# Kernel tuning notes

Measured on AMD Instinct MI355X. Metric: run time of the kernel, lower is better.

Reference implementation:

```python
import jax, jax.numpy as jnp
import numpy as np

DEPTH, DIM, DFF, VOCAB = 4, 512, 2048, 4096
EPS = 1e-5

def layernorm(x, w, b):
    mu = jnp.mean(x, axis=-1, keepdims=True)
    var = jnp.mean((x - mu) ** 2, axis=-1, keepdims=True)
    return (x - mu) * jax.lax.rsqrt(var + EPS) * w + b

def sconv(x, phazor_c, last_conv_c):
    # x: [B,L,dim] real; phazor_c, last_conv_c: [dim] complex
    B, L, D = x.shape
    r = jnp.abs(phazor_c)
    p = jnp.tanh(r) * jnp.exp(1j * jnp.angle(phazor_c))          # [dim]
    prog = p[None, :] ** jnp.arange(L, dtype=jnp.float32)[:, None]  # [L,dim]
    filt_fft = jnp.fft.fft(prog, n=2 * L, axis=0)                # [2L,dim]
    x_fft = jnp.fft.fft(x.astype(jnp.complex64), n=2 * L, axis=1)  # [B,2L,dim]
    conv = jnp.fft.ifft(filt_fft[None] * x_fft, axis=1)[:, :L]   # [B,L,dim]
    conv = conv + last_conv_c[None, None, :] * prog[None] * p[None, None, :]
    return conv.real.astype(x.dtype)

def setup_inputs() -> dict:
    key = jax.random.key(0)
    ks = jax.random.split(key, 20)
    f32 = jnp.float32
    inp = {}
    inp['x'] = jax.random.normal(ks[0], (2, 4096, VOCAB), dtype=f32)
    inp['Win'] = jax.random.normal(ks[1], (DIM, VOCAB), dtype=f32) * VOCAB ** -0.5
    inp['bin'] = jnp.zeros((DIM,), f32)
    inp['ln1_w'] = jnp.ones((DEPTH, DIM), f32)
    inp['ln1_b'] = jnp.zeros((DEPTH, DIM), f32)
    # phazor init: exp(2*pi*i*arange/dim)*|randn|
    ang = 2 * np.pi * jnp.arange(DIM, dtype=f32) / DIM
    mag = jnp.abs(jax.random.normal(ks[2], (DEPTH, DIM), dtype=f32))
    inp['phz_re'] = mag * jnp.cos(ang)[None]
    inp['phz_im'] = mag * jnp.sin(ang)[None]
    inp['lc_re'] = jax.random.normal(ks[3], (DEPTH, DIM), dtype=f32)
    inp['lc_im'] = jax.random.normal(ks[4], (DEPTH, DIM), dtype=f32)
    inp['sc_lin'] = jnp.ones((DEPTH, DIM), f32)
    inp['ln2_w'] = jnp.ones((DEPTH, DIM), f32)
    inp['ln2_b'] = jnp.zeros((DEPTH, DIM), f32)
    inp['W1'] = jax.random.normal(ks[5], (DEPTH, DFF, DIM), dtype=f32) * DIM ** -0.5
    inp['b1'] = jnp.zeros((DEPTH, DFF), f32)
    inp['W2'] = jax.random.normal(ks[6], (DEPTH, DIM, DFF), dtype=f32) * DFF ** -0.5
    inp['b2'] = jnp.zeros((DEPTH, DIM), f32)
    inp['lnl_w'] = jnp.ones((DIM,), f32)
    inp['lnl_b'] = jnp.zeros((DIM,), f32)
    inp['Wout'] = jax.random.normal(ks[7], (VOCAB, DIM), dtype=f32) * DIM ** -0.5
    inp['bout'] = jnp.zeros((VOCAB,), f32)
    return inp

def _forward(x, Win, bin, ln1_w, ln1_b, phz_re, phz_im, lc_re, lc_im, sc_lin,
             ln2_w, ln2_b, W1, b1, W2, b2, lnl_w, lnl_b, Wout, bout):
    h = jnp.einsum('blv,dv->bld', x, Win) + bin  # token_in

    def body(h, p):
        l1w, l1b, pr, pi, lr, li, scl, l2w, l2b, w1, b1_, w2, b2_ = p
        y = jax.nn.silu(layernorm(h, l1w, l1b))
        y = sconv(y, pr + 1j * pi, lr + 1j * li)
        h = h + y * scl
        y = layernorm(h, l2w, l2b)
        y = jax.nn.silu(jnp.einsum('bld,fd->blf', y, w1) + b1_)
        y = jnp.einsum('blf,df->bld', y, w2) + b2_
        return h + y, None

    xs = (ln1_w, ln1_b, phz_re, phz_im, lc_re, lc_im, sc_lin,
          ln2_w, ln2_b, W1, b1, W2, b2)
    h, _ = jax.lax.scan(body, h, xs)
    h = layernorm(h, lnl_w, lnl_b)
    return jnp.einsum('bld,vd->blv', h, Wout) + bout

def reference(x, Win, bin, ln1_w, ln1_b, phz_re, phz_im, lc_re, lc_im, sc_lin,
              ln2_w, ln2_b, W1, b1, W2, b2, lnl_w, lnl_b, Wout, bout):
    return _forward(x, Win, bin, ln1_w, ln1_b, phz_re, phz_im, lc_re, lc_im,
                    sc_lin, ln2_w, ln2_b, W1, b1, W2, b2, lnl_w, lnl_b, Wout, bout)
```

## Files before the change

### kernel.cpp

```cpp
#include <hip/hip_runtime.h>
#include <hip/hip_bf16.h>
#include <cstdint>
#include <cstddef>

#define DEPTH 4
#define DIM 512
#define DFF 2048
#define VOCAB 4096
#define NB 2
#define LSEQ 4096
#define MR (NB*LSEQ)
#define EPSL 1e-5f
#define NC 256
#define TCH 16

typedef __attribute__((ext_vector_type(8))) short  s8v;
typedef __attribute__((ext_vector_type(4))) float  f4v;
typedef __attribute__((ext_vector_type(8))) __bf16 bf8v;

__device__ __forceinline__ unsigned short f2b(float f) {
  union { float f; unsigned int u; } v; v.f = f;
  unsigned int r = v.u + 0x7FFFu + ((v.u >> 16) & 1u);
  return (unsigned short)(r >> 16);
}

__device__ __forceinline__ void gld16(const void* g, void* l) {
  __builtin_amdgcn_global_load_lds(
      (const __attribute__((address_space(1))) unsigned int*)(uintptr_t)g,
      (__attribute__((address_space(3))) unsigned int*)(uintptr_t)l,
      16, 0, 0);
}

template<int N> __device__ __forceinline__ void wvm() {
  if constexpr (N == 8)      asm volatile("s_waitcnt vmcnt(8)" ::: "memory");
  else if constexpr (N == 6) asm volatile("s_waitcnt vmcnt(6)" ::: "memory");
  else if constexpr (N == 4) asm volatile("s_waitcnt vmcnt(4)" ::: "memory");
  else if constexpr (N == 3) asm volatile("s_waitcnt vmcnt(3)" ::: "memory");
  else                       asm volatile("s_waitcnt vmcnt(0)" ::: "memory");
}

__device__ __forceinline__ void wred64(float& s, float& s2) {
#pragma unroll
  for (int off = 32; off; off >>= 1) { s += __shfl_xor(s, off, 64); s2 += __shfl_xor(s2, off, 64); }
}

__global__ void __launch_bounds__(256) cvt_f32_bf16(
    const float* __restrict__ in, unsigned short* __restrict__ out, int n8)
{
  int i = blockIdx.x * 256 + threadIdx.x;
  if (i >= n8) return;
  const f4v* p = (const f4v*)(in + (size_t)i * 8);
  f4v a = p[0], b = p[1];
  s8v o;
  o[0]=(short)f2b(a[0]); o[1]=(short)f2b(a[1]); o[2]=(short)f2b(a[2]); o[3]=(short)f2b(a[3]);
  o[4]=(short)f2b(b[0]); o[5]=(short)f2b(b[1]); o[6]=(short)f2b(b[2]); o[7]=(short)f2b(b[3]);
  *(s8v*)(out + (size_t)i * 8) = o;
}

__device__ __forceinline__ void phz2p(float re, float im, float& pre, float& pim) {
  float r = sqrtf(re * re + im * im);
  float t = (r > 1e-20f) ? (tanhf(r) / r) : 1.0f;
  pre = t * re; pim = t * im;
}

__global__ void __launch_bounds__(512) ln_scan(
    const float* __restrict__ h,
    const float* __restrict__ lnw, const float* __restrict__ lnb,
    const float* __restrict__ pr, const float* __restrict__ pi,
    float* __restrict__ y, float* __restrict__ stA)
{
  __shared__ float ls[TCH][DIM];
  const int d = threadIdx.x;
  const int c = blockIdx.x, b = blockIdx.y;
  const size_t rbase = ((size_t)b * LSEQ + (size_t)c * TCH) * DIM + d;
#pragma unroll 4
  for (int j = 0; j < TCH; ++j) ls[j][d] = h[rbase + (size_t)j * DIM];
  __syncthreads();
  const int wave = threadIdx.x >> 6, lane = threadIdx.x & 63;
  const int c8 = lane * 8;
  f4v w0 = *(const f4v*)(lnw + c8), w1 = *(const f4v*)(lnw + c8 + 4);
  f4v b0 = *(const f4v*)(lnb + c8), b1 = *(const f4v*)(lnb + c8 + 4);
#pragma unroll
  for (int jj = 0; jj < 2; ++jj) {
    int j = wave * 2 + jj;
    f4v v0 = *(const f4v*)&ls[j][c8];
    f4v v1 = *(const f4v*)&ls[j][c8 + 4];
    float s = 0.f, s2 = 0.f;
#pragma unroll
    for (int q = 0; q < 4; ++q) { s += v0[q]; s2 += v0[q]*v0[q]; s += v1[q]; s2 += v1[q]*v1[q]; }
    wred64(s, s2);
    float mu = s * (1.f / DIM);
    float rs = rsqrtf(s2 * (1.f / DIM) - mu * mu + EPSL);
    f4v o0, o1;
#pragma unroll
    for (int q = 0; q < 4; ++q) {
      float a = (v0[q] - mu) * rs * w0[q] + b0[q];
      o0[q] = a / (1.f + __expf(-a));
      float e = (v1[q] - mu) * rs * w1[q] + b1[q];
      o1[q] = e / (1.f + __expf(-e));
    }
    *(f4v*)&ls[j][c8]     = o0;
    *(f4v*)&ls[j][c8 + 4] = o1;
    size_t yo = ((size_t)b * LSEQ + (size_t)c * TCH + j) * DIM + c8;
    *(f4v*)(y + yo)     = o0;
    *(f4v*)(y + yo + 4) = o1;
  }
  __syncthreads();
  float pre, pim; phz2p(pr[d], pi[d], pre, pim);
  float sre = 0.f, sim = 0.f;
#pragma unroll
  for (int j = 0; j < TCH; ++j) {
    float xv = ls[j][d];
    float nre = fmaf(pre, sre, fmaf(-pim, sim, xv));
    float nim = fmaf(pre, sim, pim * sre);
    sre = nre; sim = nim;
  }
  size_t o = (((size_t)b * NC + c) * DIM + d) * 2;
  stA[o] = sre; stA[o + 1] = sim;
}

__global__ void __launch_bounds__(256) scan_b(
    const float* __restrict__ stA, float* __restrict__ carry,
    const float* __restrict__ pr, const float* __restrict__ pi,
    const float* __restrict__ lcr, const float* __restrict__ lci)
{
  int idx = blockIdx.x * 256 + threadIdx.x;
  int b = idx >> 9, d = idx & (DIM - 1);
  float pre, pim; phz2p(pr[d], pi[d], pre, pim);
  float qre = pre, qim = pim;
#pragma unroll
  for (int t = 0; t < 4; ++t) { float nr = qre*qre - qim*qim; float ni = 2.f*qre*qim; qre = nr; qim = ni; }
  float cre = lcr[d], cim = lci[d];
  const size_t base = (size_t)b * NC * DIM * 2 + (size_t)d * 2;
  for (int c0 = 0; c0 < NC; c0 += 8) {
    float ar[8], ai[8];
#pragma unroll
    for (int k = 0; k < 8; ++k) {
      size_t o = base + (size_t)(c0 + k) * DIM * 2;
      ar[k] = stA[o]; ai[k] = stA[o + 1];
    }
#pragma unroll
    for (int k = 0; k < 8; ++k) {
      size_t o = base + (size_t)(c0 + k) * DIM * 2;
      carry[o] = cre; carry[o + 1] = cim;
      float nr = fmaf(qre, cre, fmaf(-qim, cim, ar[k]));
      float ni = fmaf(qre, cim, fmaf(qim, cre, ai[k]));
      cre = nr; cim = ni;
    }
  }
}

__global__ void __launch_bounds__(512) scan_c_ln2(
    const float* __restrict__ y, float* __restrict__ h, const float* __restrict__ carry,
    const float* __restrict__ pr, const float* __restrict__ pi,
    const float* __restrict__ scl,
    const float* __restrict__ lnw, const float* __restrict__ lnb,
    unsigned short* __restrict__ yb)
{
  __shared__ float ls[TCH][DIM];
  const int d = threadIdx.x;
  const int c = blockIdx.x, b = blockIdx.y;
  float pre, pim; phz2p(pr[d], pi[d], pre, pim);
  size_t co = (((size_t)b * NC + c) * DIM + d) * 2;
  float sre = carry[co], sim = carry[co + 1];
  const float sc = scl[d];
  const size_t rbase = ((size_t)b * LSEQ + (size_t)c * TCH) * DIM + d;
#pragma unroll 4
  for (int j = 0; j < TCH; ++j) {
    size_t o = rbase + (size_t)j * DIM;
    float xv = y[o];
    float nre = fmaf(pre, sre, fmaf(-pim, sim, xv));
    float nim = fmaf(pre, sim, pim * sre);
    sre = nre; sim = nim;
    float hv = h[o] + sre * sc;
    h[o] = hv;
    ls[j][d] = hv;
  }
  __syncthreads();
  const int wave = threadIdx.x >> 6, lane = threadIdx.x & 63;
  const int c8 = lane * 8;
  f4v w0 = *(const f4v*)(lnw + c8), w1 = *(const f4v*)(lnw + c8 + 4);
  f4v b0 = *(const f4v*)(lnb + c8), b1 = *(const f4v*)(lnb + c8 + 4);
#pragma unroll
  for (int jj = 0; jj < 2; ++jj) {
    int j = wave * 2 + jj;
    f4v v0 = *(const f4v*)&ls[j][c8];
    f4v v1 = *(const f4v*)&ls[j][c8 + 4];
    float s = 0.f, s2 = 0.f;
#pragma unroll
    for (int q = 0; q < 4; ++q) { s += v0[q]; s2 += v0[q]*v0[q]; s += v1[q]; s2 += v1[q]*v1[q]; }
    wred64(s, s2);
    float mu = s * (1.f / DIM);
    float rs = rsqrtf(s2 * (1.f / DIM) - mu * mu + EPSL);
    s8v o;
#pragma unroll
    for (int q = 0; q < 4; ++q) {
      o[q]     = (short)f2b((v0[q] - mu) * rs * w0[q] + b0[q]);
      o[4 + q] = (short)f2b((v1[q] - mu) * rs * w1[q] + b1[q]);
    }
    *(s8v*)(yb + ((size_t)b * LSEQ + (size_t)c * TCH + j) * DIM + c8) = o;
  }
}

__global__ void __launch_bounds__(512) ln_final(
    const float* __restrict__ h,
    const float* __restrict__ lnw, const float* __restrict__ lnb,
    unsigned short* __restrict__ yb)
{
  __shared__ float ls[TCH][DIM];
  const int d = threadIdx.x;
  const int c = blockIdx.x, b = blockIdx.y;
  const size_t rbase = ((size_t)b * LSEQ + (size_t)c * TCH) * DIM + d;
#pragma unroll 4
  for (int j = 0; j < TCH; ++j) ls[j][d] = h[rbase + (size_t)j * DIM];
  __syncthreads();
  const int wave = threadIdx.x >> 6, lane = threadIdx.x & 63;
  const int c8 = lane * 8;
  f4v w0 = *(const f4v*)(lnw + c8), w1 = *(const f4v*)(lnw + c8 + 4);
  f4v b0 = *(const f4v*)(lnb + c8), b1 = *(const f4v*)(lnb + c8 + 4);
#pragma unroll
  for (int jj = 0; jj < 2; ++jj) {
    int j = wave * 2 + jj;
    f4v v0 = *(const f4v*)&ls[j][c8];
    f4v v1 = *(const f4v*)&ls[j][c8 + 4];
    float s = 0.f, s2 = 0.f;
#pragma unroll
    for (int q = 0; q < 4; ++q) { s += v0[q]; s2 += v0[q]*v0[q]; s += v1[q]; s2 += v1[q]*v1[q]; }
    wred64(s, s2);
    float mu = s * (1.f / DIM);
    float rs = rsqrtf(s2 * (1.f / DIM) - mu * mu + EPSL);
    s8v o;
#pragma unroll
    for (int q = 0; q < 4; ++q) {
      o[q]     = (short)f2b((v0[q] - mu) * rs * w0[q] + b0[q]);
      o[4 + q] = (short)f2b((v1[q] - mu) * rs * w1[q] + b1[q]);
    }
    *(s8v*)(yb + ((size_t)b * LSEQ + (size_t)c * TCH + j) * DIM + c8) = o;
  }
}

template<int EPI, int BN>
__global__ void __launch_bounds__(256, BN == 64 ? 4 : 3) gemm_p(
    const unsigned short* __restrict__ A, const unsigned short* __restrict__ Bm,
    const float* __restrict__ bias,
    float* __restrict__ Cf, unsigned short* __restrict__ Cb,
    int N, int K, int lda, int ldb)
{
  constexpr int WN  = BN / 2;
  constexpr int NJ  = WN / 16;
  constexpr int VPT = 2 + BN / 64;
  __shared__ unsigned short As[3][128 * 32];
  __shared__ unsigned short Bs[3][BN * 32];
  const int tid  = threadIdx.x;
  const int lane = tid & 63, wave = tid >> 6;
  const int wm = wave >> 1, wn = wave & 1;
  const int fr = lane & 15, fq = lane >> 4;

  int bx, by;
  {
    int gx = gridDim.x;
    int nwg = gx * gridDim.y;
    int b = blockIdx.y * gx + blockIdx.x;
    int lid = (b & 7) * (nwg >> 3) + (b >> 3);
    bx = lid % gx; by = lid / gx;
  }
  const int m0 = by * 128, n0 = bx * BN;
  const int nkt = K >> 5;

  f4v acc[4][NJ];
#pragma unroll
  for (int i = 0; i < 4; ++i)
#pragma unroll
    for (int j = 0; j < NJ; ++j) acc[i][j] = (f4v){0.f, 0.f, 0.f, 0.f};

  const int row2 = tid >> 2, col2 = (tid & 3) << 3;
  auto stage = [&](int buf, int kt) {
    const unsigned short* Ab = A  + (size_t)m0 * lda + kt * 32;
    const unsigned short* Bb = Bm + (size_t)n0 * ldb + kt * 32;
    gld16(Ab + (size_t)row2 * lda + col2,        &As[buf][tid * 8]);
    gld16(Ab + (size_t)(row2 + 64) * lda + col2, &As[buf][(256 + tid) * 8]);
    gld16(Bb + (size_t)row2 * ldb + col2,        &Bs[buf][tid * 8]);
    if constexpr (BN == 128)
      gld16(Bb + (size_t)(row2 + 64) * ldb + col2, &Bs[buf][(256 + tid) * 8]);
  };

  stage(0, 0);
  stage(1, 1);

  int b0 = 0, b1 = 1, b2 = 2;
  for (int kt = 0; kt < nkt; ++kt) {
    bool pf = (kt + 2 < nkt);
    if (pf) stage(b2, kt + 2);
    if (pf)                    wvm<2 * VPT>();
    else if (kt + 1 < nkt)     wvm<VPT>();
    else                       wvm<0>();
    __builtin_amdgcn_s_barrier();
    __builtin_amdgcn_sched_barrier(0);
    bf8v av[4], bv[NJ];
#pragma unroll
    for (int i = 0; i < 4; ++i)
      av[i] = *(const bf8v*)&As[b0][(wm * 64 + i * 16 + fr) * 32 + fq * 8];
#pragma unroll
    for (int j = 0; j < NJ; ++j)
      bv[j] = *(const bf8v*)&Bs[b0][(wn * WN + j * 16 + fr) * 32 + fq * 8];
#pragma unroll
    for (int i = 0; i < 4; ++i)
#pragma unroll
      for (int j = 0; j < NJ; ++j)
        acc[i][j] = __builtin_amdgcn_mfma_f32_16x16x32_bf16(av[i], bv[j], acc[i][j], 0, 0, 0);
    __builtin_amdgcn_sched_barrier(0);
    __builtin_amdgcn_s_barrier();
    int t = b0; b0 = b1; b1 = b2; b2 = t;
  }

#pragma unroll
  for (int j = 0; j < NJ; ++j) {
    const int col = n0 + wn * WN + j * 16 + fr;
    const float bsv = bias[col];
#pragma unroll
    for (int i = 0; i < 4; ++i) {
#pragma unroll
      for (int r = 0; r < 4; ++r) {
        const int row = m0 + wm * 64 + i * 16 + fq * 4 + r;
        const size_t off = (size_t)row * N + col;
        float v = acc[i][j][r] + bsv;
        if constexpr (EPI == 0) {
          Cf[off] = v;
        } else if constexpr (EPI == 1) {
          float sv = v / (1.f + __expf(-v));
          Cb[off] = f2b(sv);
        } else {
          Cf[off] = Cf[off] + v;
        }
      }
    }
  }
}

extern "C" void kernel_launch(void* const* d_in, const int* in_sizes, int n_in,
                              void* d_out, int out_size, void* d_ws, size_t ws_size,
                              hipStream_t stream)
{
  (void)in_sizes; (void)n_in; (void)out_size; (void)ws_size;
  const float* x    = (const float*)d_in[0];
  const float* Win  = (const float*)d_in[1];
  const float* bin  = (const float*)d_in[2];
  const float* ln1w = (const float*)d_in[3];
  const float* ln1b = (const float*)d_in[4];
  const float* phzr = (const float*)d_in[5];
  const float* phzi = (const float*)d_in[6];
  const float* lcr  = (const float*)d_in[7];
  const float* lci  = (const float*)d_in[8];
  const float* scl  = (const float*)d_in[9];
  const float* ln2w = (const float*)d_in[10];
  const float* ln2b = (const float*)d_in[11];
  const float* W1   = (const float*)d_in[12];
  const float* b1   = (const float*)d_in[13];
  const float* W2   = (const float*)d_in[14];
  const float* b2   = (const float*)d_in[15];
  const float* lnlw = (const float*)d_in[16];
  const float* lnlb = (const float*)d_in[17];
  const float* Wout = (const float*)d_in[18];
  const float* bout = (const float*)d_in[19];

  char* wsp = (char*)d_ws;
  auto alloc = [&](size_t bytes) { char* p = wsp; wsp += (bytes + 255) & ~(size_t)255; return p; };
  float*          h     = (float*)alloc((size_t)MR * DIM * 4);
  float*          y     = (float*)alloc((size_t)MR * DIM * 4);
  unsigned short* yb    = (unsigned short*)alloc((size_t)MR * DIM * 2);
  unsigned short* Winb  = (unsigned short*)alloc((size_t)DIM * VOCAB * 2);
  unsigned short* W1b   = (unsigned short*)alloc((size_t)DEPTH * DFF * DIM * 2);
  unsigned short* W2b   = (unsigned short*)alloc((size_t)DEPTH * DIM * DFF * 2);
  unsigned short* Woutb = (unsigned short*)alloc((size_t)VOCAB * DIM * 2);
  float*          stA   = (float*)alloc((size_t)NB * NC * DIM * 2 * 4);
  float*          carry = (float*)alloc((size_t)NB * NC * DIM * 2 * 4);

  unsigned short* xb   = (unsigned short*)d_out;
  unsigned short* act1 = (unsigned short*)d_out;

  dim3 blk(256);
  dim3 fblk(512);
  dim3 fgrid(NC, NB);
  cvt_f32_bf16<<<dim3(((size_t)MR * VOCAB) / 2048), blk, 0, stream>>>(x, xb, (int)(((size_t)MR * VOCAB) / 8));
  cvt_f32_bf16<<<dim3((DIM * VOCAB) / 2048), blk, 0, stream>>>(Win, Winb, DIM * VOCAB / 8);
  cvt_f32_bf16<<<dim3((DEPTH * DFF * DIM) / 2048), blk, 0, stream>>>(W1, W1b, DEPTH * DFF * DIM / 8);
  cvt_f32_bf16<<<dim3((DEPTH * DFF * DIM) / 2048), blk, 0, stream>>>(W2, W2b, DEPTH * DIM * DFF / 8);
  cvt_f32_bf16<<<dim3((VOCAB * DIM) / 2048), blk, 0, stream>>>(Wout, Woutb, VOCAB * DIM / 8);

  gemm_p<0, 64><<<dim3(DIM / 64, MR / 128), blk, 0, stream>>>(
      xb, Winb, bin, h, nullptr, DIM, VOCAB, VOCAB, VOCAB);
  ln_scan<<<fgrid, fblk, 0, stream>>>(h, ln1w, ln1b, phzr, phzi, y, stA);

  for (int l = 0; l < DEPTH; ++l) {
    scan_b<<<dim3((NB * DIM) / 256), blk, 0, stream>>>(stA, carry, phzr + l * DIM, phzi + l * DIM,
                                                       lcr + l * DIM, lci + l * DIM);
    scan_c_ln2<<<fgrid, fblk, 0, stream>>>(y, h, carry, phzr + l * DIM, phzi + l * DIM,
                                           scl + l * DIM, ln2w + l * DIM, ln2b + l * DIM, yb);
    gemm_p<1, 128><<<dim3(DFF / 128, MR / 128), blk, 0, stream>>>(
        yb, W1b + (size_t)l * DFF * DIM, b1 + l * DFF, nullptr, act1, DFF, DIM, DIM, DIM);
    gemm_p<2, 64><<<dim3(DIM / 64, MR / 128), blk, 0, stream>>>(
        act1, W2b + (size_t)l * DIM * DFF, b2 + l * DIM, h, nullptr, DIM, DFF, DFF, DFF);
    if (l < DEPTH - 1) {
      ln_scan<<<fgrid, fblk, 0, stream>>>(h, ln1w + (l + 1) * DIM, ln1b + (l + 1) * DIM,
                                          phzr + (l + 1) * DIM, phzi + (l + 1) * DIM, y, stA);
    }
  }
  ln_final<<<fgrid, fblk, 0, stream>>>(h, lnlw, lnlb, yb);
  gemm_p<0, 128><<<dim3(VOCAB / 128, MR / 128), blk, 0, stream>>>(
      yb, Woutb, bout, (float*)d_out, nullptr, VOCAB, DIM, DIM, DIM);
}
```

Baseline: 584.3 us.

## Fuse fp32-to-bf16 input conversion into token-in GEMM loading fp32 tiles

```diff
diff --git a/kernel.cpp b/kernel.cpp
--- a/kernel.cpp
+++ b/kernel.cpp
@@ -32,8 +32,10 @@
 }
 
 template<int N> __device__ __forceinline__ void wvm() {
-  if constexpr (N == 8)      asm volatile("s_waitcnt vmcnt(8)" ::: "memory");
+  if constexpr (N == 10)     asm volatile("s_waitcnt vmcnt(10)" ::: "memory");
+  else if constexpr (N == 8) asm volatile("s_waitcnt vmcnt(8)" ::: "memory");
   else if constexpr (N == 6) asm volatile("s_waitcnt vmcnt(6)" ::: "memory");
+  else if constexpr (N == 5) asm volatile("s_waitcnt vmcnt(5)" ::: "memory");
   else if constexpr (N == 4) asm volatile("s_waitcnt vmcnt(4)" ::: "memory");
   else if constexpr (N == 3) asm volatile("s_waitcnt vmcnt(3)" ::: "memory");
   else                       asm volatile("s_waitcnt vmcnt(0)" ::: "memory");
@@ -332,6 +334,100 @@
         } else {
           Cf[off] = Cf[off] + v;
         }
+      }
+    }
+  }
+}
+
+__global__ void __launch_bounds__(256, 2) gemm_tok(
+    const float* __restrict__ A, const unsigned short* __restrict__ Bm,
+    const float* __restrict__ bias, float* __restrict__ Cf, int N, int K)
+{
+  constexpr int VPT = 5;
+  __shared__ float          Asf[3][128 * 32];
+  __shared__ unsigned short Bs[3][64 * 32];
+  const int tid  = threadIdx.x;
+  const int lane = tid & 63, wave = tid >> 6;
+  const int wm = wave >> 1, wn = wave & 1;
+  const int fr = lane & 15, fq = lane >> 4;
+
+  int bx, by;
+  {
+    int gx = gridDim.x;
+    int nwg = gx * gridDim.y;
+    int b = blockIdx.y * gx + blockIdx.x;
+    int lid = (b & 7) * (nwg >> 3) + (b >> 3);
+    bx = lid % gx; by = lid / gx;
+  }
+  const int m0 = by * 128, n0 = bx * 64;
+  const int nkt = K >> 5;
+
+  f4v acc[4][2];
+#pragma unroll
+  for (int i = 0; i < 4; ++i)
+#pragma unroll
+    for (int j = 0; j < 2; ++j) acc[i][j] = (f4v){0.f, 0.f, 0.f, 0.f};
+
+  const int row2 = tid >> 2, col2 = (tid & 3) << 3;
+  auto stage = [&](int buf, int kt) {
+    const float* Ab = A + (size_t)m0 * K + kt * 32;
+    const unsigned short* Bb = Bm + (size_t)n0 * K + kt * 32;
+#pragma unroll
+    for (int q = 0; q < 4; ++q) {
+      int s = q * 256 + tid;
+      int row = s >> 3;
+      int c4  = (s & 7) ^ (row & 7);
+      gld16(Ab + (size_t)row * K + c4 * 4, &Asf[buf][s * 4]);
+    }
+    gld16(Bb + (size_t)row2 * K + col2, &Bs[buf][tid * 8]);
+  };
+
+  stage(0, 0);
+  stage(1, 1);
+
+  int b0 = 0, b1 = 1, b2 = 2;
+  for (int kt = 0; kt < nkt; ++kt) {
+    bool pf = (kt + 2 < nkt);
+    if (pf) stage(b2, kt + 2);
+    if (pf)                    wvm<2 * VPT>();
+    else if (kt + 1 < nkt)     wvm<VPT>();
+    else                       wvm<0>();
+    __builtin_amdgcn_s_barrier();
+    __builtin_amdgcn_sched_barrier(0);
+    bf8v av[4], bv[2];
+#pragma unroll
+    for (int i = 0; i < 4; ++i) {
+      int arow = wm * 64 + i * 16 + fr;
+      int g0 = arow * 8 + ((fq * 2) ^ (arow & 7));
+      int g1 = g0 ^ 1;
+      f4v lo = *(const f4v*)&Asf[b0][g0 * 4];
+      f4v hi = *(const f4v*)&Asf[b0][g1 * 4];
+#pragma unroll
+      for (int q = 0; q < 4; ++q) { av[i][q] = (__bf16)lo[q]; av[i][4 + q] = (__bf16)hi[q]; }
+    }
+#pragma unroll
+    for (int j = 0; j < 2; ++j)
+      bv[j] = *(const bf8v*)&Bs[b0][(wn * 32 + j * 16 + fr) * 32 + fq * 8];
+#pragma unroll
+    for (int i = 0; i < 4; ++i)
+#pragma unroll
+      for (int j = 0; j < 2; ++j)
+        acc[i][j] = __builtin_amdgcn_mfma_f32_16x16x32_bf16(av[i], bv[j], acc[i][j], 0, 0, 0);
+    __builtin_amdgcn_sched_barrier(0);
+    __builtin_amdgcn_s_barrier();
+    int t = b0; b0 = b1; b1 = b2; b2 = t;
+  }
+
+#pragma unroll
+  for (int j = 0; j < 2; ++j) {
+    const int col = n0 + wn * 32 + j * 16 + fr;
+    const float bsv = bias[col];
+#pragma unroll
+    for (int i = 0; i < 4; ++i) {
+#pragma unroll
+      for (int r = 0; r < 4; ++r) {
+        const int row = m0 + wm * 64 + i * 16 + fq * 4 + r;
+        Cf[(size_t)row * N + col] = acc[i][j][r] + bsv;
       }
     }
   }
@@ -375,20 +471,17 @@
   float*          stA   = (float*)alloc((size_t)NB * NC * DIM * 2 * 4);
   float*          carry = (float*)alloc((size_t)NB * NC * DIM * 2 * 4);
 
-  unsigned short* xb   = (unsigned short*)d_out;
   unsigned short* act1 = (unsigned short*)d_out;
 
   dim3 blk(256);
   dim3 fblk(512);
   dim3 fgrid(NC, NB);
-  cvt_f32_bf16<<<dim3(((size_t)MR * VOCAB) / 2048), blk, 0, stream>>>(x, xb, (int)(((size_t)MR * VOCAB) / 8));
   cvt_f32_bf16<<<dim3((DIM * VOCAB) / 2048), blk, 0, stream>>>(Win, Winb, DIM * VOCAB / 8);
   cvt_f32_bf16<<<dim3((DEPTH * DFF * DIM) / 2048), blk, 0, stream>>>(W1, W1b, DEPTH * DFF * DIM / 8);
   cvt_f32_bf16<<<dim3((DEPTH * DFF * DIM) / 2048), blk, 0, stream>>>(W2, W2b, DEPTH * DIM * DFF / 8);
   cvt_f32_bf16<<<dim3((VOCAB * DIM) / 2048), blk, 0, stream>>>(Wout, Woutb, VOCAB * DIM / 8);
 
-  gemm_p<0, 64><<<dim3(DIM / 64, MR / 128), blk, 0, stream>>>(
-      xb, Winb, bin, h, nullptr, DIM, VOCAB, VOCAB, VOCAB);
+  gemm_tok<<<dim3(DIM / 64, MR / 128), blk, 0, stream>>>(x, Winb, bin, h, DIM, VOCAB);
   ln_scan<<<fgrid, fblk, 0, stream>>>(h, ln1w, ln1b, phzr, phzi, y, stA);
 
   for (int l = 0; l < DEPTH; ++l) {
```

New measurement: 608.4 us. 1.04x slower.

## Split-K the input projection GEMM and fuse all bf16 conversions into one kernel

Applied to the files above, without the earlier changes.

```diff
diff --git a/kernel.cpp b/kernel.cpp
--- a/kernel.cpp
+++ b/kernel.cpp
@@ -44,17 +44,32 @@
   for (int off = 32; off; off >>= 1) { s += __shfl_xor(s, off, 64); s2 += __shfl_xor(s2, off, 64); }
 }
 
-__global__ void __launch_bounds__(256) cvt_f32_bf16(
-    const float* __restrict__ in, unsigned short* __restrict__ out, int n8)
-{
-  int i = blockIdx.x * 256 + threadIdx.x;
-  if (i >= n8) return;
-  const f4v* p = (const f4v*)(in + (size_t)i * 8);
+#define NX8 4194304
+#define NW8  262144
+#define N18  524288
+#define N28  524288
+#define NO8  262144
+__global__ void __launch_bounds__(256) cvt_all(
+    const float* __restrict__ x,  const float* __restrict__ Win,
+    const float* __restrict__ W1, const float* __restrict__ W2,
+    const float* __restrict__ Wout,
+    unsigned short* __restrict__ xb,  unsigned short* __restrict__ Winb,
+    unsigned short* __restrict__ W1b, unsigned short* __restrict__ W2b,
+    unsigned short* __restrict__ Woutb)
+{
+  long i = (long)blockIdx.x * 256 + threadIdx.x;
+  const float* src; unsigned short* dst; long j;
+  if (i < NX8)                         { src = x;    dst = xb;    j = i; }
+  else if (i < NX8 + NW8)              { src = Win;  dst = Winb;  j = i - NX8; }
+  else if (i < NX8 + NW8 + N18)        { src = W1;   dst = W1b;   j = i - NX8 - NW8; }
+  else if (i < NX8 + NW8 + N18 + N28)  { src = W2;   dst = W2b;   j = i - NX8 - NW8 - N18; }
+  else                                 { src = Wout; dst = Woutb; j = i - NX8 - NW8 - N18 - N28; }
+  const f4v* p = (const f4v*)(src + j * 8);
   f4v a = p[0], b = p[1];
   s8v o;
   o[0]=(short)f2b(a[0]); o[1]=(short)f2b(a[1]); o[2]=(short)f2b(a[2]); o[3]=(short)f2b(a[3]);
   o[4]=(short)f2b(b[0]); o[5]=(short)f2b(b[1]); o[6]=(short)f2b(b[2]); o[7]=(short)f2b(b[3]);
-  *(s8v*)(out + (size_t)i * 8) = o;
+  *(s8v*)(dst + j * 8) = o;
 }
 
 __device__ __forceinline__ void phz2p(float re, float im, float& pre, float& pim) {
@@ -244,7 +259,7 @@
     const unsigned short* __restrict__ A, const unsigned short* __restrict__ Bm,
     const float* __restrict__ bias,
     float* __restrict__ Cf, unsigned short* __restrict__ Cb,
-    int N, int K, int lda, int ldb)
+    int N, int Keff, int lda, int ldb)
 {
   constexpr int WN  = BN / 2;
   constexpr int NJ  = WN / 16;
@@ -255,6 +270,7 @@
   const int lane = tid & 63, wave = tid >> 6;
   const int wm = wave >> 1, wn = wave & 1;
   const int fr = lane & 15, fq = lane >> 4;
+  const int bz = blockIdx.z;
 
   int bx, by;
   {
@@ -265,7 +281,8 @@
     bx = lid % gx; by = lid / gx;
   }
   const int m0 = by * 128, n0 = bx * BN;
-  const int nkt = K >> 5;
+  const int koff = bz * Keff;
+  const int nkt = Keff >> 5;
 
   f4v acc[4][NJ];
 #pragma unroll
@@ -275,8 +292,8 @@
 
   const int row2 = tid >> 2, col2 = (tid & 3) << 3;
   auto stage = [&](int buf, int kt) {
-    const unsigned short* Ab = A  + (size_t)m0 * lda + kt * 32;
-    const unsigned short* Bb = Bm + (size_t)n0 * ldb + kt * 32;
+    const unsigned short* Ab = A  + (size_t)m0 * lda + koff + kt * 32;
+    const unsigned short* Bb = Bm + (size_t)n0 * ldb + koff + kt * 32;
     gld16(Ab + (size_t)row2 * lda + col2,        &As[buf][tid * 8]);
     gld16(Ab + (size_t)(row2 + 64) * lda + col2, &As[buf][(256 + tid) * 8]);
     gld16(Bb + (size_t)row2 * ldb + col2,        &Bs[buf][tid * 8]);
@@ -313,10 +330,11 @@
     int t = b0; b0 = b1; b1 = b2; b2 = t;
   }
 
+  const size_t pbase = (EPI == 3) ? (size_t)bz * MR * N : 0;
 #pragma unroll
   for (int j = 0; j < NJ; ++j) {
     const int col = n0 + wn * WN + j * 16 + fr;
-    const float bsv = bias[col];
+    const float bsv = (EPI == 3) ? 0.f : bias[col];
 #pragma unroll
     for (int i = 0; i < 4; ++i) {
 #pragma unroll
@@ -329,12 +347,30 @@
         } else if constexpr (EPI == 1) {
           float sv = v / (1.f + __expf(-v));
           Cb[off] = f2b(sv);
+        } else if constexpr (EPI == 2) {
+          Cf[off] = Cf[off] + v;
         } else {
-          Cf[off] = Cf[off] + v;
+          Cf[pbase + off] = v;
         }
       }
     }
   }
+}
+
+template<int NP, int RES>
+__global__ void __launch_bounds__(256) reduce_sk(
+    const float* __restrict__ parts, const float* __restrict__ bias,
+    float* __restrict__ out)
+{
+  size_t i = ((size_t)blockIdx.x * 256 + threadIdx.x) * 4;
+  const size_t st = (size_t)MR * DIM;
+  f4v v = *(const f4v*)(parts + i);
+#pragma unroll
+  for (int p = 1; p < NP; ++p) v += *(const f4v*)(parts + (size_t)p * st + i);
+  int c = (int)(i & (DIM - 1));
+  v += *(const f4v*)(bias + c);
+  if (RES) v += *(const f4v*)(out + i);
+  *(f4v*)(out + i) = v;
 }
 
 extern "C" void kernel_launch(void* const* d_in, const int* in_sizes, int n_in,
@@ -375,20 +411,20 @@
   float*          stA   = (float*)alloc((size_t)NB * NC * DIM * 2 * 4);
   float*          carry = (float*)alloc((size_t)NB * NC * DIM * 2 * 4);
 
-  unsigned short* xb   = (unsigned short*)d_out;
-  unsigned short* act1 = (unsigned short*)d_out;
+  unsigned short* xb    = (unsigned short*)d_out;
+  unsigned short* act1  = (unsigned short*)d_out;
+  float*          parts = (float*)((char*)d_out + ((size_t)64 << 20));
 
   dim3 blk(256);
   dim3 fblk(512);
   dim3 fgrid(NC, NB);
-  cvt_f32_bf16<<<dim3(((size_t)MR * VOCAB) / 2048), blk, 0, stream>>>(x, xb, (int)(((size_t)MR * VOCAB) / 8));
-  cvt_f32_bf16<<<dim3((DIM * VOCAB) / 2048), blk, 0, stream>>>(Win, Winb, DIM * VOCAB / 8);
-  cvt_f32_bf16<<<dim3((DEPTH * DFF * DIM) / 2048), blk, 0, stream>>>(W1, W1b, DEPTH * DFF * DIM / 8);
-  cvt_f32_bf16<<<dim3((DEPTH * DFF * DIM) / 2048), blk, 0, stream>>>(W2, W2b, DEPTH * DIM * DFF / 8);
-  cvt_f32_bf16<<<dim3((VOCAB * DIM) / 2048), blk, 0, stream>>>(Wout, Woutb, VOCAB * DIM / 8);
-
-  gemm_p<0, 64><<<dim3(DIM / 64, MR / 128), blk, 0, stream>>>(
-      xb, Winb, bin, h, nullptr, DIM, VOCAB, VOCAB, VOCAB);
+  cvt_all<<<dim3((NX8 + NW8 + N18 + N28 + NO8) / 256), blk, 0, stream>>>(
+      x, Win, W1, W2, Wout, xb, Winb, W1b, W2b, Woutb);
+
+  gemm_p<3, 128><<<dim3(DIM / 128, MR / 128, 2), blk, 0, stream>>>(
+      xb, Winb, nullptr, parts, nullptr, DIM, VOCAB / 2, VOCAB, VOCAB);
+  reduce_sk<2, 0><<<dim3(MR * DIM / 1024), blk, 0, stream>>>(parts, bin, h);
+
   ln_scan<<<fgrid, fblk, 0, stream>>>(h, ln1w, ln1b, phzr, phzi, y, stA);
 
   for (int l = 0; l < DEPTH; ++l) {
@@ -396,9 +432,9 @@
                                                        lcr + l * DIM, lci + l * DIM);
     scan_c_ln2<<<fgrid, fblk, 0, stream>>>(y, h, carry, phzr + l * DIM, phzi + l * DIM,
                                            scl + l * DIM, ln2w + l * DIM, ln2b + l * DIM, yb);
-    gemm_p<1, 128><<<dim3(DFF / 128, MR / 128), blk, 0, stream>>>(
+    gemm_p<1, 128><<<dim3(DFF / 128, MR / 128, 1), blk, 0, stream>>>(
         yb, W1b + (size_t)l * DFF * DIM, b1 + l * DFF, nullptr, act1, DFF, DIM, DIM, DIM);
-    gemm_p<2, 64><<<dim3(DIM / 64, MR / 128), blk, 0, stream>>>(
+    gemm_p<2, 64><<<dim3(DIM / 64, MR / 128, 1), blk, 0, stream>>>(
         act1, W2b + (size_t)l * DIM * DFF, b2 + l * DIM, h, nullptr, DIM, DFF, DFF, DFF);
     if (l < DEPTH - 1) {
       ln_scan<<<fgrid, fblk, 0, stream>>>(h, ln1w + (l + 1) * DIM, ln1b + (l + 1) * DIM,
@@ -406,6 +442,6 @@
     }
   }
   ln_final<<<fgrid, fblk, 0, stream>>>(h, lnlw, lnlb, yb);
-  gemm_p<0, 128><<<dim3(VOCAB / 128, MR / 128), blk, 0, stream>>>(
+  gemm_p<0, 128><<<dim3(VOCAB / 128, MR / 128, 1), blk, 0, stream>>>(
       yb, Woutb, bout, (float*)d_out, nullptr, VOCAB, DIM, DIM, DIM);
 }
```

Result: no change. 573.8 us (-1.8%).
